# Kernel tuning notes

Hardware: AMD Instinct MI355X
Metric: run time of the kernel (lower is better)

The kernel has to match this reference:

```python
import jax, jax.numpy as jnp
import numpy as np

N_NODES = 100000
N_EDGES = 600000
NODE_DIM = 128
EDGE_DIM = 16
OUT_DIM = 128


def setup_inputs() -> dict:
    key = jax.random.key(0)
    k1, k2, k3, k4 = jax.random.split(key, 4)
    x = jax.random.normal(k1, (N_NODES, NODE_DIM), dtype=jnp.float32)
    edge_index = jax.random.randint(k2, (2, N_EDGES), 0, N_NODES, dtype=jnp.int64)
    edge_attr = jax.random.normal(k3, (N_EDGES, EDGE_DIM), dtype=jnp.float32)
    in_dim = 2 * NODE_DIM + EDGE_DIM
    # Linear layer params (Kaiming-uniform-like scale)
    lim = 1.0 / np.sqrt(in_dim)
    W = jax.random.uniform(k4, (in_dim, OUT_DIM), minval=-lim, maxval=lim, dtype=jnp.float32)
    b = jnp.zeros((OUT_DIM,), dtype=jnp.float32)
    return {"x": x, "edge_index": edge_index, "edge_attr": edge_attr, "W": W, "b": b}


def reference(x, edge_index, edge_attr, W, b):
    # h_ij = Linear([h_i, h_j, x_ij])
    h_i = x[edge_index[0]]            # [E, node_dim]
    h_j = x[edge_index[1]]            # [E, node_dim]
    # Split the GEMM over the concat blocks to avoid materializing [E, 2D+F]
    W_i, W_j, W_e = W[:NODE_DIM], W[NODE_DIM:2 * NODE_DIM], W[2 * NODE_DIM:]
    out = h_i @ W_i + h_j @ W_j + edge_attr @ W_e + b
    return out  # [E, out_dim]
```

## Files before the change

### kernel.cpp

```cpp
#include <hip/hip_runtime.h>
#include <cstdint>
#include <cstddef>

#define NE 600000
#define NN 100000

typedef __attribute__((ext_vector_type(8)))  __bf16         bf16x8;
typedef __attribute__((ext_vector_type(16))) float          f32x16;
typedef __attribute__((ext_vector_type(8)))  unsigned short u16x8;
typedef __attribute__((ext_vector_type(2)))  float          f32x2;

__device__ inline unsigned short f2bf(float f) {
    unsigned int u = __builtin_bit_cast(unsigned int, f);
    u += 0x7fffu + ((u >> 16) & 1u);
    return (unsigned short)(u >> 16);
}

__global__ void pack_w(const float* __restrict__ W, unsigned short* __restrict__ Wp) {
    int t = blockIdx.x * 256 + threadIdx.x;
    if (t >= 272 * 128) return;
    int k = t >> 7, col = t & 127;
    Wp[((k >> 3) * 128 + col) * 8 + (k & 7)] = f2bf(W[t]);
}

__global__ void cvt_x(const float* __restrict__ x, unsigned short* __restrict__ xb) {
    size_t t = (size_t)(blockIdx.x * 256 + threadIdx.x) * 8;
    float4 a = *(const float4*)(x + t);
    float4 b = *(const float4*)(x + t + 4);
    u16x8 o;
    o[0] = f2bf(a.x); o[1] = f2bf(a.y); o[2] = f2bf(a.z); o[3] = f2bf(a.w);
    o[4] = f2bf(b.x); o[5] = f2bf(b.y); o[6] = f2bf(b.z); o[7] = f2bf(b.w);
    *(u16x8*)(xb + t) = o;
}


__global__ __launch_bounds__(256, 2) void node_mm(
    const unsigned short* __restrict__ xb,
    const unsigned short* __restrict__ Wp,
    float* __restrict__ Y,
    float* __restrict__ Z)
{
    const int lane = threadIdx.x & 63;
    const int wave = threadIdx.x >> 6;
    const int r = lane & 31;
    const int h = lane >> 5;
    const int nb = (blockIdx.x * 4 + wave) * 32;
    if (nb >= NN) return;

    const bf16x8* Wg = (const bf16x8*)Wp;
    f32x16 accY[4], accZ[4];
#pragma unroll
    for (int t = 0; t < 4; ++t)
#pragma unroll
        for (int i = 0; i < 16; ++i) { accY[t][i] = 0.f; accZ[t][i] = 0.f; }

#pragma unroll
    for (int S = 0; S < 8; ++S) {
        const int kb = 2 * S + h;
        bf16x8 a = *(const bf16x8*)(xb + (size_t)(nb + r) * 128 + kb * 8);
#pragma unroll
        for (int t = 0; t < 4; ++t) {
            accY[t] = __builtin_amdgcn_mfma_f32_32x32x16_bf16(
                          a, Wg[kb * 128 + t * 32 + r],        accY[t], 0, 0, 0);
            accZ[t] = __builtin_amdgcn_mfma_f32_32x32x16_bf16(
                          a, Wg[(16 + kb) * 128 + t * 32 + r], accZ[t], 0, 0, 0);
        }
    }

#pragma unroll
    for (int t = 0; t < 4; ++t)
#pragma unroll
        for (int i = 0; i < 16; ++i) {
            int row = (i & 3) + 8 * (i >> 2) + 4 * h;
            Y[(size_t)(nb + row) * 128 + t * 32 + r] = accY[t][i];
            Z[(size_t)(nb + row) * 128 + t * 32 + r] = accZ[t][i];
        }
}

__global__ __launch_bounds__(256, 5) void edge_combine(
    const float* __restrict__ Y,
    const float* __restrict__ Z,
    const int*   __restrict__ ei,
    const float* __restrict__ ea,
    const float* __restrict__ W,
    const float* __restrict__ bias,
    float* __restrict__ out)
{
    const int lane = threadIdx.x & 63;
    const int w = (blockIdx.x * 256 + threadIdx.x) >> 6;
    if (w >= NE / 64) return;
    const int ebase = w * 64;

    float wex[16], wey[16];
#pragma unroll
    for (int k = 0; k < 16; ++k) {
        f32x2 t = *(const f32x2*)(W + (size_t)(256 + k) * 128 + 2 * lane);
        wex[k] = t.x; wey[k] = t.y;
    }
    const f32x2 bv = *(const f32x2*)(bias + 2 * lane);

    const int srcv = ei[ebase + lane];
    const int dstv = ei[NE + ebase + lane];
    const float* eab = ea + (size_t)ebase * 16;

#pragma unroll 2
    for (int jo = 0; jo < 16; ++jo) {
        float eag = __builtin_nontemporal_load(eab + jo * 64 + lane);
#pragma unroll
        for (int ji = 0; ji < 4; ++ji) {
            const int j = jo * 4 + ji;
            const int s = __builtin_amdgcn_readlane(srcv, j);
            const int d = __builtin_amdgcn_readlane(dstv, j);
            f32x2 y = *(const f32x2*)(Y + ((size_t)s << 7) + 2 * lane);
            f32x2 z = *(const f32x2*)(Z + ((size_t)d << 7) + 2 * lane);

            float ax = bv.x, ay = bv.y;
#pragma unroll
            for (int k = 0; k < 16; ++k) {
                int eb = __builtin_amdgcn_readlane(
                             __builtin_bit_cast(int, eag), ji * 16 + k);
                float e = __builtin_bit_cast(float, eb);
                ax = fmaf(e, wex[k], ax);
                ay = fmaf(e, wey[k], ay);
            }
            f32x2 o;
            o.x = ax + y.x + z.x;
            o.y = ay + y.y + z.y;
            __builtin_nontemporal_store(
                o, (f32x2*)(out + ((size_t)(ebase + j) << 7) + 2 * lane));
        }
    }
}


#define WAIT_VM(n) do { asm volatile("" ::: "memory");                      \
                        __builtin_amdgcn_s_waitcnt(0x0F70 | (n));           \
                        asm volatile("" ::: "memory"); } while (0)

__global__ __launch_bounds__(256, 2) void edge_mm2(
    const unsigned short* __restrict__ xb,
    const unsigned short* __restrict__ Wp,
    const int* __restrict__ ei,
    const float* __restrict__ ea,
    const float* __restrict__ bias,
    float* __restrict__ out)
{
    __shared__ __attribute__((aligned(16))) unsigned short Abuf[4][2][32][128];

    const int lane = threadIdx.x & 63;
    const int wave = threadIdx.x >> 6;
    const int r  = lane & 31;
    const int h  = lane >> 5;
    const int g4 = lane >> 4;
    const int sl = lane & 15;
    const int ebase = blockIdx.x * 128 + wave * 32;
    if (ebase >= NE) return;
    const int e = ebase + r;

#pragma unroll
    for (int i = 0; i < 8; ++i) {
        int row = 4 * i + g4;
        int nidx = ei[ebase + row];
        const unsigned short* gs = xb + (size_t)nidx * 128 + ((sl ^ (row & 15)) << 3);
        __builtin_amdgcn_global_load_lds(
            (const __attribute__((address_space(1))) void*)gs,
            (__attribute__((address_space(3))) void*)&Abuf[wave][0][4 * i][0],
            16, 0, 0);
    }
#pragma unroll
    for (int i = 0; i < 8; ++i) {
        int row = 4 * i + g4;
        int nidx = ei[NE + ebase + row];
        const unsigned short* gs = xb + (size_t)nidx * 128 + ((sl ^ (row & 15)) << 3);
        __builtin_amdgcn_global_load_lds(
            (const __attribute__((address_space(1))) void*)gs,
            (__attribute__((address_space(3))) void*)&Abuf[wave][1][4 * i][0],
            16, 0, 0);
    }

    const float4* ae = (const float4*)(ea + (size_t)e * 16);
    float4 p = ae[2 * h], q = ae[2 * h + 1];

    f32x16 acc[4];
#pragma unroll
    for (int t = 0; t < 4; ++t)
#pragma unroll
        for (int i = 0; i < 16; ++i) acc[t][i] = 0.f;

    const bf16x8* Wg = (const bf16x8*)Wp;
    const int rm = r & 15;

    WAIT_VM(8);
#pragma unroll
    for (int S = 0; S < 8; ++S) {
        int kb = 2 * S + h;
        bf16x8 a = *(const bf16x8*)&Abuf[wave][0][r][(kb ^ rm) << 3];
#pragma unroll
        for (int t = 0; t < 4; ++t) {
            bf16x8 b = Wg[kb * 128 + t * 32 + r];
            acc[t] = __builtin_amdgcn_mfma_f32_32x32x16_bf16(a, b, acc[t], 0, 0, 0);
        }
    }

    WAIT_VM(0);
#pragma unroll
    for (int S = 0; S < 8; ++S) {
        int kb = 2 * S + h;
        bf16x8 a = *(const bf16x8*)&Abuf[wave][1][r][(kb ^ rm) << 3];
#pragma unroll
        for (int t = 0; t < 4; ++t) {
            bf16x8 b = Wg[(16 + kb) * 128 + t * 32 + r];
            acc[t] = __builtin_amdgcn_mfma_f32_32x32x16_bf16(a, b, acc[t], 0, 0, 0);
        }
    }

    {
        u16x8 o;
        o[0] = f2bf(p.x); o[1] = f2bf(p.y); o[2] = f2bf(p.z); o[3] = f2bf(p.w);
        o[4] = f2bf(q.x); o[5] = f2bf(q.y); o[6] = f2bf(q.z); o[7] = f2bf(q.w);
        bf16x8 a = __builtin_bit_cast(bf16x8, o);
#pragma unroll
        for (int t = 0; t < 4; ++t) {
            bf16x8 b = Wg[(32 + h) * 128 + t * 32 + r];
            acc[t] = __builtin_amdgcn_mfma_f32_32x32x16_bf16(a, b, acc[t], 0, 0, 0);
        }
    }

    float* orow = out + (size_t)ebase * 128;
#pragma unroll
    for (int t = 0; t < 4; ++t) {
        float bv = bias[t * 32 + r];
#pragma unroll
        for (int i = 0; i < 16; ++i) {
            int row = (i & 3) + 8 * (i >> 2) + 4 * h;
            orow[(size_t)row * 128 + t * 32 + r] = acc[t][i] + bv;
        }
    }
}

__global__ __launch_bounds__(256, 2) void edge_mm_fb(
    const float* __restrict__ x,
    const unsigned short* __restrict__ Wp,
    const int* __restrict__ ei,
    const float* __restrict__ ea,
    const float* __restrict__ bias,
    float* __restrict__ out)
{
    __shared__ unsigned short Wl[32 * 128 * 8];
    {
        const uint4* Wg = (const uint4*)Wp;
        uint4* Ws = (uint4*)Wl;
#pragma unroll
        for (int i = 0; i < 16; ++i)
            Ws[threadIdx.x + 256 * i] = Wg[threadIdx.x + 256 * i];
    }
    const int lane = threadIdx.x & 63;
    const int wave = threadIdx.x >> 6;
    const int r = lane & 31;
    const int h = lane >> 5;
    const long ebase = (long)blockIdx.x * 128 + wave * 32;
    __syncthreads();
    if (ebase >= NE) return;
    const int e = (int)ebase + r;
    const int src = ei[e];
    const int dst = ei[NE + e];
    f32x16 acc[4];
#pragma unroll
    for (int t = 0; t < 4; ++t)
#pragma unroll
        for (int i = 0; i < 16; ++i) acc[t][i] = 0.f;
    const bf16x8* Wv = (const bf16x8*)Wl;
#pragma unroll
    for (int ph = 0; ph < 2; ++ph) {
        int node = ph ? dst : src;
#pragma unroll
        for (int s = 0; s < 8; ++s) {
            const float4* ax = (const float4*)(x + (size_t)node * 128);
            float4 pp = ax[(2 * s + h) * 2], qq = ax[(2 * s + h) * 2 + 1];
            u16x8 o;
            o[0] = f2bf(pp.x); o[1] = f2bf(pp.y); o[2] = f2bf(pp.z); o[3] = f2bf(pp.w);
            o[4] = f2bf(qq.x); o[5] = f2bf(qq.y); o[6] = f2bf(qq.z); o[7] = f2bf(qq.w);
            bf16x8 a = __builtin_bit_cast(bf16x8, o);
            int S = ph * 8 + s;
#pragma unroll
            for (int t = 0; t < 4; ++t) {
                bf16x8 b = Wv[(2 * S + h) * 128 + t * 32 + r];
                acc[t] = __builtin_amdgcn_mfma_f32_32x32x16_bf16(a, b, acc[t], 0, 0, 0);
            }
        }
    }
    {
        const float4* ae = (const float4*)(ea + (size_t)e * 16);
        float4 pp = ae[2 * h], qq = ae[2 * h + 1];
        u16x8 o;
        o[0] = f2bf(pp.x); o[1] = f2bf(pp.y); o[2] = f2bf(pp.z); o[3] = f2bf(pp.w);
        o[4] = f2bf(qq.x); o[5] = f2bf(qq.y); o[6] = f2bf(qq.z); o[7] = f2bf(qq.w);
        bf16x8 a = __builtin_bit_cast(bf16x8, o);
        const bf16x8* Wg = (const bf16x8*)Wp;
#pragma unroll
        for (int t = 0; t < 4; ++t) {
            bf16x8 b = Wg[(32 + h) * 128 + t * 32 + r];
            acc[t] = __builtin_amdgcn_mfma_f32_32x32x16_bf16(a, b, acc[t], 0, 0, 0);
        }
    }
    float* orow = out + (size_t)ebase * 128;
#pragma unroll
    for (int t = 0; t < 4; ++t) {
        float bv = bias[t * 32 + r];
#pragma unroll
        for (int i = 0; i < 16; ++i) {
            int row = (i & 3) + 8 * (i >> 2) + 4 * h;
            orow[(size_t)row * 128 + t * 32 + r] = acc[t][i] + bv;
        }
    }
}

extern "C" void kernel_launch(void* const* d_in, const int* in_sizes, int n_in,
                              void* d_out, int out_size, void* d_ws, size_t ws_size,
                              hipStream_t stream) {
    const float* x  = (const float*)d_in[0];
    const int*   ei = (const int*)d_in[1];
    const float* ea = (const float*)d_in[2];
    const float* W  = (const float*)d_in[3];
    const float* b  = (const float*)d_in[4];
    float* out = (float*)d_out;

    unsigned short* Wp = (unsigned short*)d_ws;
    unsigned short* xb = (unsigned short*)((char*)d_ws + 69632);
    float* Yb = (float*)((char*)d_ws + 69632 + 25600000);
    float* Zb = (float*)((char*)d_ws + 69632 + 25600000 + 51200000);

    const size_t need_mid  = 69632 + (size_t)NN * 128 * 2;
    const size_t need_full = need_mid + 2ull * NN * 128 * 4;

    hipLaunchKernelGGL(pack_w, dim3(136), dim3(256), 0, stream, W, Wp);

    if (ws_size >= need_full) {
        hipLaunchKernelGGL(cvt_x, dim3(6250), dim3(256), 0, stream, x, xb);
        hipLaunchKernelGGL(node_mm, dim3(782), dim3(256), 0, stream, xb, Wp, Yb, Zb);
        hipLaunchKernelGGL(edge_combine, dim3(2344), dim3(256), 0, stream,
                           Yb, Zb, ei, ea, W, b, out);
    } else if (ws_size >= need_mid) {
        hipLaunchKernelGGL(cvt_x, dim3(6250), dim3(256), 0, stream, x, xb);
        hipLaunchKernelGGL(edge_mm2, dim3(4688), dim3(256), 0, stream,
                           xb, Wp, ei, ea, b, out);
    } else {
        hipLaunchKernelGGL(edge_mm_fb, dim3(4688), dim3(256), 0, stream,
                           x, Wp, ei, ea, b, out);
    }
}
```

Before: 525.0 us.

## Fuse bf16 conversion into node GEMM and software-pipeline edge gathers

The node GEMM now reads fp32 x directly and converts it to bf16 in registers, so the separate cvt_x launch and its intermediate buffer are gone. The edge combine kernel loads all edge attributes up front and keeps an 8-deep rotating prefetch of the gathered Y/Z rows, so the random-access latency overlaps with compute. It also packs the weights as f32x2 vector FMAs. The extra registers for the prefetch ring force occupancy down from 5 to 4 blocks, which weakens latency hiding through wave switching. The workspace layout is shrunk to match.

```diff
diff --git a/kernel.cpp b/kernel.cpp
--- a/kernel.cpp
+++ b/kernel.cpp
@@ -35,7 +35,7 @@
 
 
 __global__ __launch_bounds__(256, 2) void node_mm(
-    const unsigned short* __restrict__ xb,
+    const float* __restrict__ x,
     const unsigned short* __restrict__ Wp,
     float* __restrict__ Y,
     float* __restrict__ Z)
@@ -54,10 +54,15 @@
 #pragma unroll
         for (int i = 0; i < 16; ++i) { accY[t][i] = 0.f; accZ[t][i] = 0.f; }
 
+    const float4* ax4 = (const float4*)(x + (size_t)(nb + r) * 128);
 #pragma unroll
     for (int S = 0; S < 8; ++S) {
         const int kb = 2 * S + h;
-        bf16x8 a = *(const bf16x8*)(xb + (size_t)(nb + r) * 128 + kb * 8);
+        float4 pp = ax4[kb * 2], qq = ax4[kb * 2 + 1];
+        u16x8 o;
+        o[0] = f2bf(pp.x); o[1] = f2bf(pp.y); o[2] = f2bf(pp.z); o[3] = f2bf(pp.w);
+        o[4] = f2bf(qq.x); o[5] = f2bf(qq.y); o[6] = f2bf(qq.z); o[7] = f2bf(qq.w);
+        bf16x8 a = __builtin_bit_cast(bf16x8, o);
 #pragma unroll
         for (int t = 0; t < 4; ++t) {
             accY[t] = __builtin_amdgcn_mfma_f32_32x32x16_bf16(
@@ -77,7 +82,7 @@
         }
 }
 
-__global__ __launch_bounds__(256, 5) void edge_combine(
+__global__ __launch_bounds__(256, 4) void edge_combine(
     const float* __restrict__ Y,
     const float* __restrict__ Z,
     const int*   __restrict__ ei,
@@ -91,44 +96,50 @@
     if (w >= NE / 64) return;
     const int ebase = w * 64;
 
-    float wex[16], wey[16];
-#pragma unroll
-    for (int k = 0; k < 16; ++k) {
-        f32x2 t = *(const f32x2*)(W + (size_t)(256 + k) * 128 + 2 * lane);
-        wex[k] = t.x; wey[k] = t.y;
-    }
+    f32x2 we[16];
+#pragma unroll
+    for (int k = 0; k < 16; ++k)
+        we[k] = *(const f32x2*)(W + (size_t)(256 + k) * 128 + 2 * lane);
     const f32x2 bv = *(const f32x2*)(bias + 2 * lane);
 
     const int srcv = ei[ebase + lane];
     const int dstv = ei[NE + ebase + lane];
-    const float* eab = ea + (size_t)ebase * 16;
-
-#pragma unroll 2
-    for (int jo = 0; jo < 16; ++jo) {
-        float eag = __builtin_nontemporal_load(eab + jo * 64 + lane);
-#pragma unroll
-        for (int ji = 0; ji < 4; ++ji) {
-            const int j = jo * 4 + ji;
-            const int s = __builtin_amdgcn_readlane(srcv, j);
-            const int d = __builtin_amdgcn_readlane(dstv, j);
-            f32x2 y = *(const f32x2*)(Y + ((size_t)s << 7) + 2 * lane);
-            f32x2 z = *(const f32x2*)(Z + ((size_t)d << 7) + 2 * lane);
-
-            float ax = bv.x, ay = bv.y;
-#pragma unroll
-            for (int k = 0; k < 16; ++k) {
-                int eb = __builtin_amdgcn_readlane(
-                             __builtin_bit_cast(int, eag), ji * 16 + k);
-                float e = __builtin_bit_cast(float, eb);
-                ax = fmaf(e, wex[k], ax);
-                ay = fmaf(e, wey[k], ay);
-            }
-            f32x2 o;
-            o.x = ax + y.x + z.x;
-            o.y = ay + y.y + z.y;
-            __builtin_nontemporal_store(
-                o, (f32x2*)(out + ((size_t)(ebase + j) << 7) + 2 * lane));
-        }
+
+    int raw[16];
+#pragma unroll
+    for (int m = 0; m < 16; ++m)
+        raw[m] = __builtin_bit_cast(int,
+                     ea[(size_t)ebase * 16 + m * 64 + lane]);
+
+    f32x2 yv[8], zv[8];
+#pragma unroll
+    for (int i = 0; i < 8; ++i) {
+        int s = __builtin_amdgcn_readlane(srcv, i);
+        int d = __builtin_amdgcn_readlane(dstv, i);
+        yv[i] = *(const f32x2*)(Y + ((size_t)s << 7) + 2 * lane);
+        zv[i] = *(const f32x2*)(Z + ((size_t)d << 7) + 2 * lane);
+    }
+
+#pragma unroll
+    for (int j = 0; j < 64; ++j) {
+        const int slot = j & 7;
+        f32x2 y = yv[slot], z = zv[slot];
+        if (j + 8 < 64) {
+            int s = __builtin_amdgcn_readlane(srcv, j + 8);
+            int d = __builtin_amdgcn_readlane(dstv, j + 8);
+            yv[slot] = *(const f32x2*)(Y + ((size_t)s << 7) + 2 * lane);
+            zv[slot] = *(const f32x2*)(Z + ((size_t)d << 7) + 2 * lane);
+        }
+        f32x2 acc = bv;
+#pragma unroll
+        for (int k = 0; k < 16; ++k) {
+            float e = __builtin_bit_cast(float,
+                          __builtin_amdgcn_readlane(raw[j >> 2], (j & 3) * 16 + k));
+            acc = acc + we[k] * e;
+        }
+        f32x2 o = acc + y + z;
+        __builtin_nontemporal_store(
+            o, (f32x2*)(out + ((size_t)(ebase + j) << 7) + 2 * lane));
     }
 }
 
@@ -326,18 +337,17 @@
     float* out = (float*)d_out;
 
     unsigned short* Wp = (unsigned short*)d_ws;
+    float* Yb = (float*)((char*)d_ws + 69632);
+    float* Zb = (float*)((char*)d_ws + 69632 + 51200000);
     unsigned short* xb = (unsigned short*)((char*)d_ws + 69632);
-    float* Yb = (float*)((char*)d_ws + 69632 + 25600000);
-    float* Zb = (float*)((char*)d_ws + 69632 + 25600000 + 51200000);
 
     const size_t need_mid  = 69632 + (size_t)NN * 128 * 2;
-    const size_t need_full = need_mid + 2ull * NN * 128 * 4;
+    const size_t need_full = 69632 + 2ull * NN * 128 * 4;
 
     hipLaunchKernelGGL(pack_w, dim3(136), dim3(256), 0, stream, W, Wp);
 
     if (ws_size >= need_full) {
-        hipLaunchKernelGGL(cvt_x, dim3(6250), dim3(256), 0, stream, x, xb);
-        hipLaunchKernelGGL(node_mm, dim3(782), dim3(256), 0, stream, xb, Wp, Yb, Zb);
+        hipLaunchKernelGGL(node_mm, dim3(782), dim3(256), 0, stream, x, Wp, Yb, Zb);
         hipLaunchKernelGGL(edge_combine, dim3(2344), dim3(256), 0, stream,
                            Yb, Zb, ei, ea, W, b, out);
     } else if (ws_size >= need_mid) {
```

Result: faster. 503.7 us (-4.1%).
